# Optimization experiments

Hardware: AMD Instinct MI355X
Metric: run time of the kernel (lower is better)

The kernel has to match this reference:

```python
import jax, jax.numpy as jnp
import numpy as np

HID = 32      # STGAT hidden_dim
HEADS = 8
NHID = HID // HEADS  # per-head hidden = 4
NEG_SLOPE = 0.2


def lstm_layer(x, Wih, Whh, bih, bhh):
    # x: (BN, T, H_in); torch gate order i, f, g, o
    BN = x.shape[0]
    H = Whh.shape[1]
    b = bih + bhh

    def step(carry, xt):
        h, c = carry
        z = xt @ Wih.T + h @ Whh.T + b
        i, f, g, o = jnp.split(z, 4, axis=-1)
        c = jax.nn.sigmoid(f) * c + jax.nn.sigmoid(i) * jnp.tanh(g)
        h = jax.nn.sigmoid(o) * jnp.tanh(c)
        return (h, c), h

    h0 = jnp.zeros((BN, H), x.dtype)
    _, ys = jax.lax.scan(step, (h0, h0), jnp.swapaxes(x, 0, 1))
    return jnp.swapaxes(ys, 0, 1)  # (BN, T, H)


def setup_inputs():
    key = jax.random.key(0)
    ks = jax.random.split(key, 16)
    B, N, T_in, F_in = 8, 300, 12, 3
    T_out, F_out = 12, 3
    X = jax.random.normal(ks[0], (B, N, T_in, F_in), jnp.float32)
    adj = (jax.random.uniform(ks[1], (N, N)) < 0.05).astype(jnp.float32)
    A_hat = jnp.maximum(adj, jnp.eye(N, dtype=jnp.float32))  # self-loops

    def init(k, shape, fan):
        return jax.random.normal(k, shape, jnp.float32) / np.float32(np.sqrt(fan))

    W_gat = init(ks[2], (HID, F_in), F_in)          # linear (no bias)
    a_attn = init(ks[3], (2 * NHID,), 2 * NHID)     # attn (no bias), flattened (1, 2*nhid)
    W_ih0 = init(ks[4], (4 * HID, HID), HID)
    W_hh0 = init(ks[5], (4 * HID, HID), HID)
    b_ih0 = init(ks[6], (4 * HID,), HID)
    b_hh0 = init(ks[7], (4 * HID,), HID)
    W_ih1 = init(ks[8], (4 * HID, HID), HID)
    W_hh1 = init(ks[9], (4 * HID, HID), HID)
    b_ih1 = init(ks[10], (4 * HID,), HID)
    b_hh1 = init(ks[11], (4 * HID,), HID)
    fc_W = init(ks[12], (F_out * T_out, HID), HID)
    fc_b = init(ks[13], (F_out * T_out,), HID)
    return {"A_hat": A_hat, "X": X, "W_gat": W_gat, "a_attn": a_attn,
            "W_ih0": W_ih0, "W_hh0": W_hh0, "b_ih0": b_ih0, "b_hh0": b_hh0,
            "W_ih1": W_ih1, "W_hh1": W_hh1, "b_ih1": b_ih1, "b_hh1": b_hh1,
            "fc_W": fc_W, "fc_b": fc_b}


def reference(A_hat, X, W_gat, a_attn, W_ih0, W_hh0, b_ih0, b_hh0,
              W_ih1, W_hh1, b_ih1, b_hh1, fc_W, fc_b):
    B, N, T, F = X.shape
    T_out = fc_W.shape[0] // F  # nums_feature_output == F here

    # --- GAT, vectorized over (batch, timestep) ---
    # g: (B, N, T, HEADS, NHID)
    g = (X @ W_gat.T).reshape(B, N, T, HEADS, NHID)
    a_l, a_r = a_attn[:NHID], a_attn[NHID:]
    # attn(g_concat) = a_l . g_i + a_r . g_j  (exact split of the concat+linear)
    gl = jnp.einsum('bithd,d->bith', g, a_l)
    gr = jnp.einsum('bjthd,d->bjth', g, a_r)
    e = jax.nn.leaky_relu(gl[:, :, None] + gr[:, None, :], NEG_SLOPE)  # (B,i,j,T,H)
    mask = (A_hat == 0)[None, :, :, None, None]
    e = jnp.where(mask, -jnp.inf, e)
    a = jax.nn.softmax(e, axis=2)  # softmax over j (dim=1 of the (i,j,h) tensor)
    h_gat = jnp.einsum('bijth,bjthd->bithd', a, g).reshape(B, N, T, HID)

    # --- 2-layer LSTM over time, per (b, n) sequence ---
    lstm_in = h_gat.reshape(B * N, T, HID)
    h1 = lstm_layer(lstm_in, W_ih0, W_hh0, b_ih0, b_hh0)
    h2 = lstm_layer(h1, W_ih1, W_hh1, b_ih1, b_hh1)
    h_last = h2[:, -1, :]  # (B*N, HID)

    out = h_last @ fc_W.T + fc_b
    return out.reshape(B, N, T_out, F)
```

## Files before the change

kernel.cpp:

```cpp
#include <hip/hip_runtime.h>

typedef __attribute__((ext_vector_type(8))) short s8v;
typedef __attribute__((ext_vector_type(4))) float f4v;

__device__ __forceinline__ float sgm(float x) { return 1.f / (1.f + __expf(-x)); }
__device__ __forceinline__ float tanh_fast(float x) {
    float e = __expf(-2.f * fabsf(x));
    float t = (1.f - e) / (1.f + e);
    return copysignf(t, x);
}
__device__ __forceinline__ void bsplit(float x, short& hi, short& lo) {
    unsigned u = __float_as_uint(x);
    unsigned hb = u & 0xffff0000u;
    hi = (short)(hb >> 16);
    float r = x - __uint_as_float(hb);
    lo = (short)(__float_as_uint(r) >> 16);
}

__global__ void k_nbr(const float* __restrict__ A, const float* __restrict__ Wg,
                      const float* __restrict__ aat,
                      int* __restrict__ cnt, int* __restrict__ idx,
                      float* __restrict__ walr)
{
    int i = blockIdx.x;
    int lane = threadIdx.x;
    if (i == 0 && lane < 48) {
        int h = lane / 6, q = lane - h*6;
        int cc = q % 3; bool right = q >= 3;
        float acc = 0.f;
        #pragma unroll
        for (int dd = 0; dd < 4; dd++)
            acc += aat[right ? 4+dd : dd] * Wg[(h*4+dd)*3 + cc];
        walr[lane] = acc;
    }
    int c = 0;
    for (int j0 = 0; j0 < 300; j0 += 64) {
        int j = j0 + lane;
        bool p = (j < 300) && (A[i*300 + j] != 0.f);
        unsigned long long m = __ballot(p);
        if (p) {
            int pos = __popcll(m & ((1ull << lane) - 1ull));
            if (c + pos < 64) idx[i*64 + c + pos] = j;
        }
        c += __popcll(m);
    }
    if (c > 64) c = 64;
    if (lane == 0) cnt[i] = c;
}

__global__ __launch_bounds__(256, 4) void k_attn2(
    const float* __restrict__ X, const float* __restrict__ Wg,
    const int* __restrict__ cnt, const int* __restrict__ idx,
    const float* __restrict__ walr, float* __restrict__ hgat)
{
    int u = blockIdx.x * 4 + (threadIdx.x >> 6);
    int lane = threadIdx.x & 63;
    int h = lane >> 3, j8 = lane & 7, d = j8 & 3;
    int seq = u / 12, t = u - seq*12;
    int b = seq / 300, i = seq - b*300;

    const float* wv = walr + h*6;
    float wal0 = wv[0], wal1 = wv[1], wal2 = wv[2];
    float war0 = wv[3], war1 = wv[4], war2 = wv[5];
    const float* wp = Wg + (h*4+d)*3;
    float wp0 = wp[0], wp1 = wp[1], wp2 = wp[2];

    int c = cnt[i];
    int jj[8];
    #pragma unroll
    for (int q = 0; q < 8; q++) jj[q] = idx[i*64 + q*8 + j8];

    const float* Xb = X + (size_t)b*300*36 + t*3;
    const float* Xi = Xb + i*36;
    float x0 = Xi[0], x1 = Xi[1], x2 = Xi[2];
    float gl = x0*wal0 + x1*wal1 + x2*wal2;

    float m = -1e30f, s = 0.f, a0 = 0.f, a1 = 0.f, a2 = 0.f;
    for (int q = 0; q*8 + j8 < c; q++) {
        int j = jj[q];
        const float* Xj = Xb + j*36;
        float y0 = Xj[0], y1 = Xj[1], y2 = Xj[2];
        float e = gl + y0*war0 + y1*war1 + y2*war2;
        e = e > 0.f ? e : 0.2f*e;
        if (e > m) {
            float sc = __expf(m - e);
            s = s*sc + 1.f;
            a0 = a0*sc + y0; a1 = a1*sc + y1; a2 = a2*sc + y2;
            m = e;
        } else {
            float w = __expf(e - m);
            s += w;
            a0 += w*y0; a1 += w*y1; a2 += w*y2;
        }
    }
    #pragma unroll
    for (int off = 1; off <= 4; off <<= 1) {
        float m2 = __shfl_xor(m, off, 64);
        float s2 = __shfl_xor(s, off, 64);
        float b0 = __shfl_xor(a0, off, 64);
        float b1 = __shfl_xor(a1, off, 64);
        float b2 = __shfl_xor(a2, off, 64);
        float mo = fmaxf(m, m2);
        float w1 = __expf(m - mo), w2 = __expf(m2 - mo);
        s = s*w1 + s2*w2;
        a0 = a0*w1 + b0*w2; a1 = a1*w1 + b1*w2; a2 = a2*w1 + b2*w2;
        m = mo;
    }
    if (j8 < 4) {
        float o = (a0*wp0 + a1*wp1 + a2*wp2) / s;
        hgat[(size_t)u*32 + h*4 + d] = o;
    }
}

#define SQ 10

__device__ __forceinline__ void zcomp(const short* vh, const short* vl,
    const s8v (&ah)[2], const s8v (&al)[2], f4v bias, float* zdst,
    int boff, int g, int w, int n16)
{
    s8v bh0 = *(const s8v*)((const char*)vh + boff +      g*16);
    s8v bh1 = *(const s8v*)((const char*)vh + boff + 64 + g*16);
    s8v bl0 = *(const s8v*)((const char*)vl + boff +      g*16);
    s8v bl1 = *(const s8v*)((const char*)vl + boff + 64 + g*16);
    f4v acc = bias;
    acc = __builtin_amdgcn_mfma_f32_16x16x32_bf16(ah[0], bh0, acc, 0, 0, 0);
    acc = __builtin_amdgcn_mfma_f32_16x16x32_bf16(ah[1], bh1, acc, 0, 0, 0);
    acc = __builtin_amdgcn_mfma_f32_16x16x32_bf16(al[0], bh0, acc, 0, 0, 0);
    acc = __builtin_amdgcn_mfma_f32_16x16x32_bf16(al[1], bh1, acc, 0, 0, 0);
    acc = __builtin_amdgcn_mfma_f32_16x16x32_bf16(ah[0], bl0, acc, 0, 0, 0);
    acc = __builtin_amdgcn_mfma_f32_16x16x32_bf16(ah[1], bl1, acc, 0, 0, 0);
    *(f4v*)&zdst[n16*132 + w*16 + g*4] = acc;
}

__device__ __forceinline__ float cellupd(const float* zbp, int us, int uc, float& cst)
{
    float zi = zbp[us*132 + uc],      zf = zbp[us*132 + 32 + uc];
    float zg = zbp[us*132 + 64 + uc], zo = zbp[us*132 + 96 + uc];
    cst = sgm(zf)*cst + sgm(zi)*tanh_fast(zg);
    return sgm(zo)*tanh_fast(cst);
}

__global__ __launch_bounds__(512, 1) void k_lstm5(
    const float* __restrict__ hgat,
    const float* __restrict__ Wih0, const float* __restrict__ Whh0,
    const float* __restrict__ bih0, const float* __restrict__ bhh0,
    const float* __restrict__ Wih1, const float* __restrict__ Whh1,
    const float* __restrict__ bih1, const float* __restrict__ bhh1,
    const float* __restrict__ fcW,  const float* __restrict__ fcb,
    float* __restrict__ out)
{
    __shared__ __align__(16) short vh0[16*72], vl0[16*72];
    __shared__ __align__(16) short vh1[16*72], vl1[16*72];
    __shared__ __align__(16) float zb0[16*132], zb1[16*132];
    __shared__ float sh1f[SQ*32];

    const int tid = threadIdx.x;
    const int w   = tid >> 6;
    const int l   = tid & 63;
    const int n16 = l & 15;
    const int g   = l >> 4;
    const int zrow = w*16 + n16;

    s8v a0h[2], a0l[2], a1h[2], a1l[2];
    {
        const float* s00 = Wih0 + zrow*32 + g*8;
        const float* s01 = Whh0 + zrow*32 + g*8;
        const float* s10 = Wih1 + zrow*32 + g*8;
        const float* s11 = Whh1 + zrow*32 + g*8;
        #pragma unroll
        for (int j = 0; j < 8; j++) {
            short hh, ll;
            bsplit(s00[j], hh, ll); a0h[0][j]=hh; a0l[0][j]=ll;
            bsplit(s01[j], hh, ll); a0h[1][j]=hh; a0l[1][j]=ll;
            bsplit(s10[j], hh, ll); a1h[0][j]=hh; a1l[0][j]=ll;
            bsplit(s11[j], hh, ll); a1h[1][j]=hh; a1l[1][j]=ll;
        }
    }
    f4v bias0, bias1;
    #pragma unroll
    for (int r = 0; r < 4; r++) {
        int rr = w*16 + g*4 + r;
        bias0[r] = bih0[rr] + bhh0[rr];
        bias1[r] = bih1[rr] + bhh1[rr];
    }

    const int us = tid >> 5, uc = tid & 31;
    const bool upd = tid < SQ*32;
    const int seq0 = blockIdx.x * SQ;
    const int boff = n16 * 144;

    if (upd) {
        short hh, ll;
        bsplit(hgat[(size_t)(seq0+us)*384 + uc], hh, ll);
        vh0[us*72 + uc] = hh;      vl0[us*72 + uc] = ll;
        vh0[us*72 + 32 + uc] = 0;  vl0[us*72 + 32 + uc] = 0;
        vh1[us*72 + uc] = 0;       vl1[us*72 + uc] = 0;
        vh1[us*72 + 32 + uc] = 0;  vl1[us*72 + 32 + uc] = 0;
    }
    __syncthreads();

    float c0 = 0.f, c1 = 0.f;

    zcomp(vh0, vl0, a0h, a0l, bias0, zb0, boff, g, w, n16);
    __syncthreads();
    if (upd) {
        float h0v = cellupd(zb0, us, uc, c0);
        short hh, ll; bsplit(h0v, hh, ll);
        vh0[us*72 + 32 + uc] = hh;  vl0[us*72 + 32 + uc] = ll;
        vh1[us*72 + uc]      = hh;  vl1[us*72 + uc]      = ll;
        bsplit(hgat[(size_t)(seq0+us)*384 + 32 + uc], hh, ll);
        vh0[us*72 + uc] = hh;  vl0[us*72 + uc] = ll;
    }
    __syncthreads();

    for (int t = 0; t < 12; t++) {
        zcomp(vh1, vl1, a1h, a1l, bias1, zb1, boff, g, w, n16);
        if (t < 11)
            zcomp(vh0, vl0, a0h, a0l, bias0, zb0, boff, g, w, n16);
        __syncthreads();
        if (upd) {
            float h1v = cellupd(zb1, us, uc, c1);
            short hh, ll; bsplit(h1v, hh, ll);
            vh1[us*72 + 32 + uc] = hh;  vl1[us*72 + 32 + uc] = ll;
            if (t == 11) sh1f[us*32 + uc] = h1v;
            if (t < 11) {
                float h0v = cellupd(zb0, us, uc, c0);
                bsplit(h0v, hh, ll);
                vh0[us*72 + 32 + uc] = hh;  vl0[us*72 + 32 + uc] = ll;
                vh1[us*72 + uc]      = hh;  vl1[us*72 + uc]      = ll;
                if (t + 2 < 12) {
                    bsplit(hgat[(size_t)(seq0+us)*384 + (t+2)*32 + uc], hh, ll);
                    vh0[us*72 + uc] = hh;  vl0[us*72 + uc] = ll;
                }
            }
        }
        __syncthreads();
    }

    if (tid < SQ*36) {
        int s = tid / 36, r = tid - s*36;
        float acc = fcb[r];
        #pragma unroll
        for (int c4 = 0; c4 < 8; c4++) {
            float4 uv = *(const float4*)&fcW[r*32 + 4*c4];
            acc += uv.x*sh1f[s*32+4*c4+0] + uv.y*sh1f[s*32+4*c4+1]
                 + uv.z*sh1f[s*32+4*c4+2] + uv.w*sh1f[s*32+4*c4+3];
        }
        out[(seq0 + s)*36 + r] = acc;
    }
}

__device__ __forceinline__ void lstm_step_fb(
    const float* __restrict__ sWi, const float* __restrict__ sWh,
    float bzi, float bzf, float bzg, float bzo,
    const float (&xf)[32], float (&hf)[32], float& cst, int k, int lb)
{
    float zi = bzi, zf = bzf, zg = bzg, zo = bzo;
    const int sw = k & 15;
    #pragma unroll
    for (int c2 = 0; c2 < 16; c2++) {
        const int col = 2 * (c2 ^ sw);
        float xa = xf[2*c2], xb = xf[2*c2+1];
        float ha = hf[2*c2], hb = hf[2*c2+1];
        float2 wiA = *(const float2*)&sWi[(0  + k)*32 + col];
        float2 whA = *(const float2*)&sWh[(0  + k)*32 + col];
        zi += wiA.x*xa + wiA.y*xb + whA.x*ha + whA.y*hb;
        float2 wiB = *(const float2*)&sWi[(32 + k)*32 + col];
        float2 whB = *(const float2*)&sWh[(32 + k)*32 + col];
        zf += wiB.x*xa + wiB.y*xb + whB.x*ha + whB.y*hb;
        float2 wiC = *(const float2*)&sWi[(64 + k)*32 + col];
        float2 whC = *(const float2*)&sWh[(64 + k)*32 + col];
        zg += wiC.x*xa + wiC.y*xb + whC.x*ha + whC.y*hb;
        float2 wiD = *(const float2*)&sWi[(96 + k)*32 + col];
        float2 whD = *(const float2*)&sWh[(96 + k)*32 + col];
        zo += wiD.x*xa + wiD.y*xb + whD.x*ha + whD.y*hb;
    }
    float ig = sgm(zi)*tanhf(zg);
    cst = sgm(zf)*cst + ig;
    float hl = sgm(zo)*tanhf(cst);
    #pragma unroll
    for (int d = 0; d < 32; d++) hf[d] = __shfl(hl, lb + d, 64);
}

__global__ __launch_bounds__(256) void k_fused_fb(
    const float* __restrict__ A,    const float* __restrict__ X,
    const float* __restrict__ Wg,   const float* __restrict__ aat,
    const float* __restrict__ Wih0, const float* __restrict__ Whh0,
    const float* __restrict__ bih0, const float* __restrict__ bhh0,
    const float* __restrict__ Wih1, const float* __restrict__ Whh1,
    const float* __restrict__ bih1, const float* __restrict__ bhh1,
    const float* __restrict__ fcW,  const float* __restrict__ fcb,
    float* __restrict__ out)
{
    __shared__ float sW0i[4096], sW0h[4096], sW1i[4096], sW1h[4096];
    const int tid = threadIdx.x;
    for (int x2 = tid; x2 < 2048; x2 += 256) {
        int r = x2 >> 4, p = x2 & 15;
        int o = r*32 + 2*(p ^ (r & 15));
        *(float2*)&sW0i[o] = *(const float2*)&Wih0[r*32 + 2*p];
        *(float2*)&sW0h[o] = *(const float2*)&Whh0[r*32 + 2*p];
        *(float2*)&sW1i[o] = *(const float2*)&Wih1[r*32 + 2*p];
        *(float2*)&sW1h[o] = *(const float2*)&Whh1[r*32 + 2*p];
    }
    const int w   = tid >> 5;
    const int k   = tid & 31;
    const int lb  = tid & 32;
    const int seq = blockIdx.x * 8 + w;
    const int b   = seq / 300, i = seq % 300;

    int nb0 = 0, nb1 = 0, cntv = 0;
    for (int j0 = 0; j0 < 300; j0 += 32) {
        int j = j0 + k;
        bool p = (j < 300) && (A[i*300 + j] != 0.f);
        unsigned long long m64 = __ballot(p);
        unsigned mm = (unsigned)(m64 >> lb);
        while (mm) {
            int bpos = __ffs(mm) - 1;
            if ((cntv & 31) == k && cntv < 64) {
                if (cntv & 32) nb1 = j0 + bpos; else nb0 = j0 + bpos;
            }
            cntv++;
            mm &= mm - 1;
        }
    }
    if (cntv > 64) cntv = 64;

    const int dd = k & 3;
    float wg0 = Wg[k*3+0], wg1 = Wg[k*3+1], wg2 = Wg[k*3+2];
    float alv = aat[dd],   arv = aat[4+dd];
    float b0i = bih0[k]    + bhh0[k];
    float b0f = bih0[32+k] + bhh0[32+k];
    float b0g = bih0[64+k] + bhh0[64+k];
    float b0o = bih0[96+k] + bhh0[96+k];
    float b1i = bih1[k]    + bhh1[k];
    float b1f = bih1[32+k] + bhh1[32+k];
    float b1g = bih1[64+k] + bhh1[64+k];
    float b1o = bih1[96+k] + bhh1[96+k];

    __syncthreads();

    float h0f[32], h1f[32];
    #pragma unroll
    for (int d = 0; d < 32; d++) { h0f[d] = 0.f; h1f[d] = 0.f; }
    float c0 = 0.f, c1 = 0.f;
    const size_t xrow = (size_t)(b*300 + i) * 36;

    for (int t = 0; t < 12; t++) {
        float gi = wg0*X[xrow + t*3 + 0] + wg1*X[xrow + t*3 + 1]
                 + wg2*X[xrow + t*3 + 2];
        float gl = gi * alv;
        gl += __shfl_xor(gl, 1, 64);
        gl += __shfl_xor(gl, 2, 64);

        float m = -1e30f, s = 0.f, acc = 0.f;
        for (int kk = 0; kk < cntv; kk++) {
            int v = (kk & 32) ? nb1 : nb0;
            int j = __shfl(v, lb + (kk & 31), 64);
            size_t xj = (size_t)(b*300 + j) * 36 + t*3;
            float gj = wg0*X[xj+0] + wg1*X[xj+1] + wg2*X[xj+2];
            float gr = gj * arv;
            gr += __shfl_xor(gr, 1, 64);
            gr += __shfl_xor(gr, 2, 64);
            float e = gl + gr;
            e = e > 0.f ? e : 0.2f*e;
            if (e > m) {
                float sc = __expf(m - e);
                s = s*sc + 1.f; acc = acc*sc + gj; m = e;
            } else {
                float wgt = __expf(e - m);
                s += wgt; acc += wgt*gj;
            }
        }
        float x_k = acc / s;
        float xf[32];
        #pragma unroll
        for (int d = 0; d < 32; d++) xf[d] = __shfl(x_k, lb + d, 64);
        lstm_step_fb(sW0i, sW0h, b0i, b0f, b0g, b0o, xf,  h0f, c0, k, lb);
        lstm_step_fb(sW1i, sW1h, b1i, b1f, b1g, b1o, h0f, h1f, c1, k, lb);
    }

    for (int r = k; r < 36; r += 32) {
        float a2 = fcb[r];
        #pragma unroll
        for (int c2 = 0; c2 < 16; c2++) {
            float2 u = *(const float2*)&fcW[r*32 + 2*c2];
            a2 += u.x*h1f[2*c2] + u.y*h1f[2*c2+1];
        }
        out[seq*36 + r] = a2;
    }
}

extern "C" void kernel_launch(void* const* d_in, const int* in_sizes, int n_in,
                              void* d_out, int out_size, void* d_ws, size_t ws_size,
                              hipStream_t stream)
{
    const float* A    = (const float*)d_in[0];
    const float* X    = (const float*)d_in[1];
    const float* Wg   = (const float*)d_in[2];
    const float* aat  = (const float*)d_in[3];
    const float* Wih0 = (const float*)d_in[4];
    const float* Whh0 = (const float*)d_in[5];
    const float* bih0 = (const float*)d_in[6];
    const float* bhh0 = (const float*)d_in[7];
    const float* Wih1 = (const float*)d_in[8];
    const float* Whh1 = (const float*)d_in[9];
    const float* bih1 = (const float*)d_in[10];
    const float* bhh1 = (const float*)d_in[11];
    const float* fcW  = (const float*)d_in[12];
    const float* fcb  = (const float*)d_in[13];
    float* out = (float*)d_out;

    const size_t need = (320 + 300*64) * sizeof(int) + 64*sizeof(float)
                      + (size_t)2400*384*sizeof(float);
    if (ws_size >= need) {
        int*   cnt  = (int*)d_ws;
        int*   idx  = cnt + 320;
        float* walr = (float*)(idx + 300*64);
        float* hgat = walr + 64;
        k_nbr  <<<300,  64,  0, stream>>>(A, Wg, aat, cnt, idx, walr);
        k_attn2<<<7200, 256, 0, stream>>>(X, Wg, cnt, idx, walr, hgat);
        k_lstm5<<<240,  512, 0, stream>>>(hgat, Wih0, Whh0, bih0, bhh0,
                                          Wih1, Whh1, bih1, bhh1, fcW, fcb, out);
    } else {
        k_fused_fb<<<300, 256, 0, stream>>>(A, X, Wg, aat,
                                            Wih0, Whh0, bih0, bhh0,
                                            Wih1, Whh1, bih1, bhh1,
                                            fcW, fcb, out);
    }
}
```

Baseline: 44.68 us.

## Fuse neighbor build, GAT attention and LSTM into one kernel

Merges the three launches (neighbor-list build, GAT attention, LSTM) into one 240-block kernel. Each block builds neighbor lists for its 10 sequences in shared memory and computes their GAT outputs into a shared buffer, then runs the MFMA LSTM on them. This removes two kernel launches and the global round-trip of the hgat intermediate. In exchange the GAT stage now runs on only 240 blocks instead of 7200 and recomputes neighbor lists redundantly across blocks. The workspace-free fallback kernel is also removed.

```diff
diff --git a/kernel.cpp b/kernel.cpp
--- a/kernel.cpp
+++ b/kernel.cpp
@@ -15,101 +15,6 @@
     hi = (short)(hb >> 16);
     float r = x - __uint_as_float(hb);
     lo = (short)(__float_as_uint(r) >> 16);
-}
-
-__global__ void k_nbr(const float* __restrict__ A, const float* __restrict__ Wg,
-                      const float* __restrict__ aat,
-                      int* __restrict__ cnt, int* __restrict__ idx,
-                      float* __restrict__ walr)
-{
-    int i = blockIdx.x;
-    int lane = threadIdx.x;
-    if (i == 0 && lane < 48) {
-        int h = lane / 6, q = lane - h*6;
-        int cc = q % 3; bool right = q >= 3;
-        float acc = 0.f;
-        #pragma unroll
-        for (int dd = 0; dd < 4; dd++)
-            acc += aat[right ? 4+dd : dd] * Wg[(h*4+dd)*3 + cc];
-        walr[lane] = acc;
-    }
-    int c = 0;
-    for (int j0 = 0; j0 < 300; j0 += 64) {
-        int j = j0 + lane;
-        bool p = (j < 300) && (A[i*300 + j] != 0.f);
-        unsigned long long m = __ballot(p);
-        if (p) {
-            int pos = __popcll(m & ((1ull << lane) - 1ull));
-            if (c + pos < 64) idx[i*64 + c + pos] = j;
-        }
-        c += __popcll(m);
-    }
-    if (c > 64) c = 64;
-    if (lane == 0) cnt[i] = c;
-}
-
-__global__ __launch_bounds__(256, 4) void k_attn2(
-    const float* __restrict__ X, const float* __restrict__ Wg,
-    const int* __restrict__ cnt, const int* __restrict__ idx,
-    const float* __restrict__ walr, float* __restrict__ hgat)
-{
-    int u = blockIdx.x * 4 + (threadIdx.x >> 6);
-    int lane = threadIdx.x & 63;
-    int h = lane >> 3, j8 = lane & 7, d = j8 & 3;
-    int seq = u / 12, t = u - seq*12;
-    int b = seq / 300, i = seq - b*300;
-
-    const float* wv = walr + h*6;
-    float wal0 = wv[0], wal1 = wv[1], wal2 = wv[2];
-    float war0 = wv[3], war1 = wv[4], war2 = wv[5];
-    const float* wp = Wg + (h*4+d)*3;
-    float wp0 = wp[0], wp1 = wp[1], wp2 = wp[2];
-
-    int c = cnt[i];
-    int jj[8];
-    #pragma unroll
-    for (int q = 0; q < 8; q++) jj[q] = idx[i*64 + q*8 + j8];
-
-    const float* Xb = X + (size_t)b*300*36 + t*3;
-    const float* Xi = Xb + i*36;
-    float x0 = Xi[0], x1 = Xi[1], x2 = Xi[2];
-    float gl = x0*wal0 + x1*wal1 + x2*wal2;
-
-    float m = -1e30f, s = 0.f, a0 = 0.f, a1 = 0.f, a2 = 0.f;
-    for (int q = 0; q*8 + j8 < c; q++) {
-        int j = jj[q];
-        const float* Xj = Xb + j*36;
-        float y0 = Xj[0], y1 = Xj[1], y2 = Xj[2];
-        float e = gl + y0*war0 + y1*war1 + y2*war2;
-        e = e > 0.f ? e : 0.2f*e;
-        if (e > m) {
-            float sc = __expf(m - e);
-            s = s*sc + 1.f;
-            a0 = a0*sc + y0; a1 = a1*sc + y1; a2 = a2*sc + y2;
-            m = e;
-        } else {
-            float w = __expf(e - m);
-            s += w;
-            a0 += w*y0; a1 += w*y1; a2 += w*y2;
-        }
-    }
-    #pragma unroll
-    for (int off = 1; off <= 4; off <<= 1) {
-        float m2 = __shfl_xor(m, off, 64);
-        float s2 = __shfl_xor(s, off, 64);
-        float b0 = __shfl_xor(a0, off, 64);
-        float b1 = __shfl_xor(a1, off, 64);
-        float b2 = __shfl_xor(a2, off, 64);
-        float mo = fmaxf(m, m2);
-        float w1 = __expf(m - mo), w2 = __expf(m2 - mo);
-        s = s*w1 + s2*w2;
-        a0 = a0*w1 + b0*w2; a1 = a1*w1 + b1*w2; a2 = a2*w1 + b2*w2;
-        m = mo;
-    }
-    if (j8 < 4) {
-        float o = (a0*wp0 + a1*wp1 + a2*wp2) / s;
-        hgat[(size_t)u*32 + h*4 + d] = o;
-    }
 }
 
 #define SQ 10
@@ -140,8 +45,9 @@
     return sgm(zo)*tanh_fast(cst);
 }
 
-__global__ __launch_bounds__(512, 1) void k_lstm5(
-    const float* __restrict__ hgat,
+__global__ __launch_bounds__(512, 1) void k_stgat(
+    const float* __restrict__ A,    const float* __restrict__ X,
+    const float* __restrict__ Wg,   const float* __restrict__ aat,
     const float* __restrict__ Wih0, const float* __restrict__ Whh0,
     const float* __restrict__ bih0, const float* __restrict__ bhh0,
     const float* __restrict__ Wih1, const float* __restrict__ Whh1,
@@ -149,18 +55,39 @@
     const float* __restrict__ fcW,  const float* __restrict__ fcb,
     float* __restrict__ out)
 {
+    __shared__ int   snbr[SQ][64];
+    __shared__ int   scnt[SQ];
+    __shared__ float shg[SQ*384];
     __shared__ __align__(16) short vh0[16*72], vl0[16*72];
     __shared__ __align__(16) short vh1[16*72], vl1[16*72];
     __shared__ __align__(16) float zb0[16*132], zb1[16*132];
     __shared__ float sh1f[SQ*32];
 
-    const int tid = threadIdx.x;
-    const int w   = tid >> 6;
-    const int l   = tid & 63;
-    const int n16 = l & 15;
-    const int g   = l >> 4;
+    const int tid  = threadIdx.x;
+    const int w    = tid >> 6;
+    const int l    = tid & 63;
+    const int seq0 = blockIdx.x * SQ;
+
+    for (int r = w; r < SQ; r += 8) {
+        int i = (seq0 + r) % 300;
+        int c = 0;
+        for (int j0 = 0; j0 < 300; j0 += 64) {
+            int j = j0 + l;
+            bool p = (j < 300) && (A[i*300 + j] != 0.f);
+            unsigned long long m = __ballot(p);
+            if (p) {
+                int pos = __popcll(m & ((1ull << l) - 1ull));
+                if (c + pos < 64) snbr[r][c + pos] = j;
+            }
+            c += __popcll(m);
+        }
+        if (c > 64) c = 64;
+        if (l == 0) scnt[r] = c;
+    }
+
+    const int n16  = l & 15;
+    const int g    = l >> 4;
     const int zrow = w*16 + n16;
-
     s8v a0h[2], a0l[2], a1h[2], a1l[2];
     {
         const float* s00 = Wih0 + zrow*32 + g*8;
@@ -184,14 +111,76 @@
         bias1[r] = bih1[rr] + bhh1[rr];
     }
 
+    __syncthreads();
+
+    {
+        const int h = l >> 3, j8 = l & 7, d = j8 & 3;
+        float wal0=0.f, wal1=0.f, wal2=0.f, war0=0.f, war1=0.f, war2=0.f;
+        #pragma unroll
+        for (int dd = 0; dd < 4; dd++) {
+            float av = aat[dd], bv = aat[4+dd];
+            const float* wr = Wg + (h*4+dd)*3;
+            wal0 += wr[0]*av; wal1 += wr[1]*av; wal2 += wr[2]*av;
+            war0 += wr[0]*bv; war1 += wr[1]*bv; war2 += wr[2]*bv;
+        }
+        const float* wp = Wg + (h*4+d)*3;
+        float wp0 = wp[0], wp1 = wp[1], wp2 = wp[2];
+
+        for (int q = 0; q < 15; q++) {
+            int u  = w*15 + q;
+            int us = u / 12, t = u - us*12;
+            int seq = seq0 + us;
+            int b = seq / 300, i = seq - b*300;
+            int c = scnt[us];
+
+            const float* Xb = X + (size_t)b*300*36 + t*3;
+            const float* Xi = Xb + i*36;
+            float gl = Xi[0]*wal0 + Xi[1]*wal1 + Xi[2]*wal2;
+
+            float m = -1e30f, s = 0.f, a0 = 0.f, a1 = 0.f, a2 = 0.f;
+            for (int kk = j8; kk < c; kk += 8) {
+                int j = snbr[us][kk];
+                const float* Xj = Xb + j*36;
+                float y0 = Xj[0], y1 = Xj[1], y2 = Xj[2];
+                float e = gl + y0*war0 + y1*war1 + y2*war2;
+                e = e > 0.f ? e : 0.2f*e;
+                if (e > m) {
+                    float sc = __expf(m - e);
+                    s = s*sc + 1.f;
+                    a0 = a0*sc + y0; a1 = a1*sc + y1; a2 = a2*sc + y2;
+                    m = e;
+                } else {
+                    float wt = __expf(e - m);
+                    s += wt;
+                    a0 += wt*y0; a1 += wt*y1; a2 += wt*y2;
+                }
+            }
+            #pragma unroll
+            for (int off = 1; off <= 4; off <<= 1) {
+                float m2 = __shfl_xor(m, off, 64);
+                float s2 = __shfl_xor(s, off, 64);
+                float b0 = __shfl_xor(a0, off, 64);
+                float b1 = __shfl_xor(a1, off, 64);
+                float b2 = __shfl_xor(a2, off, 64);
+                float mo = fmaxf(m, m2);
+                float w1 = __expf(m - mo), w2 = __expf(m2 - mo);
+                s = s*w1 + s2*w2;
+                a0 = a0*w1 + b0*w2; a1 = a1*w1 + b1*w2; a2 = a2*w1 + b2*w2;
+                m = mo;
+            }
+            if (j8 < 4)
+                shg[us*384 + t*32 + h*4 + d] = (a0*wp0 + a1*wp1 + a2*wp2) / s;
+        }
+    }
+    __syncthreads();
+
     const int us = tid >> 5, uc = tid & 31;
     const bool upd = tid < SQ*32;
-    const int seq0 = blockIdx.x * SQ;
     const int boff = n16 * 144;
 
     if (upd) {
         short hh, ll;
-        bsplit(hgat[(size_t)(seq0+us)*384 + uc], hh, ll);
+        bsplit(shg[us*384 + uc], hh, ll);
         vh0[us*72 + uc] = hh;      vl0[us*72 + uc] = ll;
         vh0[us*72 + 32 + uc] = 0;  vl0[us*72 + 32 + uc] = 0;
         vh1[us*72 + uc] = 0;       vl1[us*72 + uc] = 0;
@@ -208,7 +197,7 @@
         short hh, ll; bsplit(h0v, hh, ll);
         vh0[us*72 + 32 + uc] = hh;  vl0[us*72 + 32 + uc] = ll;
         vh1[us*72 + uc]      = hh;  vl1[us*72 + uc]      = ll;
-        bsplit(hgat[(size_t)(seq0+us)*384 + 32 + uc], hh, ll);
+        bsplit(shg[us*384 + 32 + uc], hh, ll);
         vh0[us*72 + uc] = hh;  vl0[us*72 + uc] = ll;
     }
     __syncthreads();
@@ -229,7 +218,7 @@
                 vh0[us*72 + 32 + uc] = hh;  vl0[us*72 + 32 + uc] = ll;
                 vh1[us*72 + uc]      = hh;  vl1[us*72 + uc]      = ll;
                 if (t + 2 < 12) {
-                    bsplit(hgat[(size_t)(seq0+us)*384 + (t+2)*32 + uc], hh, ll);
+                    bsplit(shg[us*384 + (t+2)*32 + uc], hh, ll);
                     vh0[us*72 + uc] = hh;  vl0[us*72 + uc] = ll;
                 }
             }
@@ -247,146 +236,6 @@
                  + uv.z*sh1f[s*32+4*c4+2] + uv.w*sh1f[s*32+4*c4+3];
         }
         out[(seq0 + s)*36 + r] = acc;
-    }
-}
-
-__device__ __forceinline__ void lstm_step_fb(
-    const float* __restrict__ sWi, const float* __restrict__ sWh,
-    float bzi, float bzf, float bzg, float bzo,
-    const float (&xf)[32], float (&hf)[32], float& cst, int k, int lb)
-{
-    float zi = bzi, zf = bzf, zg = bzg, zo = bzo;
-    const int sw = k & 15;
-    #pragma unroll
-    for (int c2 = 0; c2 < 16; c2++) {
-        const int col = 2 * (c2 ^ sw);
-        float xa = xf[2*c2], xb = xf[2*c2+1];
-        float ha = hf[2*c2], hb = hf[2*c2+1];
-        float2 wiA = *(const float2*)&sWi[(0  + k)*32 + col];
-        float2 whA = *(const float2*)&sWh[(0  + k)*32 + col];
-        zi += wiA.x*xa + wiA.y*xb + whA.x*ha + whA.y*hb;
-        float2 wiB = *(const float2*)&sWi[(32 + k)*32 + col];
-        float2 whB = *(const float2*)&sWh[(32 + k)*32 + col];
-        zf += wiB.x*xa + wiB.y*xb + whB.x*ha + whB.y*hb;
-        float2 wiC = *(const float2*)&sWi[(64 + k)*32 + col];
-        float2 whC = *(const float2*)&sWh[(64 + k)*32 + col];
-        zg += wiC.x*xa + wiC.y*xb + whC.x*ha + whC.y*hb;
-        float2 wiD = *(const float2*)&sWi[(96 + k)*32 + col];
-        float2 whD = *(const float2*)&sWh[(96 + k)*32 + col];
-        zo += wiD.x*xa + wiD.y*xb + whD.x*ha + whD.y*hb;
-    }
-    float ig = sgm(zi)*tanhf(zg);
-    cst = sgm(zf)*cst + ig;
-    float hl = sgm(zo)*tanhf(cst);
-    #pragma unroll
-    for (int d = 0; d < 32; d++) hf[d] = __shfl(hl, lb + d, 64);
-}
-
-__global__ __launch_bounds__(256) void k_fused_fb(
-    const float* __restrict__ A,    const float* __restrict__ X,
-    const float* __restrict__ Wg,   const float* __restrict__ aat,
-    const float* __restrict__ Wih0, const float* __restrict__ Whh0,
-    const float* __restrict__ bih0, const float* __restrict__ bhh0,
-    const float* __restrict__ Wih1, const float* __restrict__ Whh1,
-    const float* __restrict__ bih1, const float* __restrict__ bhh1,
-    const float* __restrict__ fcW,  const float* __restrict__ fcb,
-    float* __restrict__ out)
-{
-    __shared__ float sW0i[4096], sW0h[4096], sW1i[4096], sW1h[4096];
-    const int tid = threadIdx.x;
-    for (int x2 = tid; x2 < 2048; x2 += 256) {
-        int r = x2 >> 4, p = x2 & 15;
-        int o = r*32 + 2*(p ^ (r & 15));
-        *(float2*)&sW0i[o] = *(const float2*)&Wih0[r*32 + 2*p];
-        *(float2*)&sW0h[o] = *(const float2*)&Whh0[r*32 + 2*p];
-        *(float2*)&sW1i[o] = *(const float2*)&Wih1[r*32 + 2*p];
-        *(float2*)&sW1h[o] = *(const float2*)&Whh1[r*32 + 2*p];
-    }
-    const int w   = tid >> 5;
-    const int k   = tid & 31;
-    const int lb  = tid & 32;
-    const int seq = blockIdx.x * 8 + w;
-    const int b   = seq / 300, i = seq % 300;
-
-    int nb0 = 0, nb1 = 0, cntv = 0;
-    for (int j0 = 0; j0 < 300; j0 += 32) {
-        int j = j0 + k;
-        bool p = (j < 300) && (A[i*300 + j] != 0.f);
-        unsigned long long m64 = __ballot(p);
-        unsigned mm = (unsigned)(m64 >> lb);
-        while (mm) {
-            int bpos = __ffs(mm) - 1;
-            if ((cntv & 31) == k && cntv < 64) {
-                if (cntv & 32) nb1 = j0 + bpos; else nb0 = j0 + bpos;
-            }
-            cntv++;
-            mm &= mm - 1;
-        }
-    }
-    if (cntv > 64) cntv = 64;
-
-    const int dd = k & 3;
-    float wg0 = Wg[k*3+0], wg1 = Wg[k*3+1], wg2 = Wg[k*3+2];
-    float alv = aat[dd],   arv = aat[4+dd];
-    float b0i = bih0[k]    + bhh0[k];
-    float b0f = bih0[32+k] + bhh0[32+k];
-    float b0g = bih0[64+k] + bhh0[64+k];
-    float b0o = bih0[96+k] + bhh0[96+k];
-    float b1i = bih1[k]    + bhh1[k];
-    float b1f = bih1[32+k] + bhh1[32+k];
-    float b1g = bih1[64+k] + bhh1[64+k];
-    float b1o = bih1[96+k] + bhh1[96+k];
-
-    __syncthreads();
-
-    float h0f[32], h1f[32];
-    #pragma unroll
-    for (int d = 0; d < 32; d++) { h0f[d] = 0.f; h1f[d] = 0.f; }
-    float c0 = 0.f, c1 = 0.f;
-    const size_t xrow = (size_t)(b*300 + i) * 36;
-
-    for (int t = 0; t < 12; t++) {
-        float gi = wg0*X[xrow + t*3 + 0] + wg1*X[xrow + t*3 + 1]
-                 + wg2*X[xrow + t*3 + 2];
-        float gl = gi * alv;
-        gl += __shfl_xor(gl, 1, 64);
-        gl += __shfl_xor(gl, 2, 64);
-
-        float m = -1e30f, s = 0.f, acc = 0.f;
-        for (int kk = 0; kk < cntv; kk++) {
-            int v = (kk & 32) ? nb1 : nb0;
-            int j = __shfl(v, lb + (kk & 31), 64);
-            size_t xj = (size_t)(b*300 + j) * 36 + t*3;
-            float gj = wg0*X[xj+0] + wg1*X[xj+1] + wg2*X[xj+2];
-            float gr = gj * arv;
-            gr += __shfl_xor(gr, 1, 64);
-            gr += __shfl_xor(gr, 2, 64);
-            float e = gl + gr;
-            e = e > 0.f ? e : 0.2f*e;
-            if (e > m) {
-                float sc = __expf(m - e);
-                s = s*sc + 1.f; acc = acc*sc + gj; m = e;
-            } else {
-                float wgt = __expf(e - m);
-                s += wgt; acc += wgt*gj;
-            }
-        }
-        float x_k = acc / s;
-        float xf[32];
-        #pragma unroll
-        for (int d = 0; d < 32; d++) xf[d] = __shfl(x_k, lb + d, 64);
-        lstm_step_fb(sW0i, sW0h, b0i, b0f, b0g, b0o, xf,  h0f, c0, k, lb);
-        lstm_step_fb(sW1i, sW1h, b1i, b1f, b1g, b1o, h0f, h1f, c1, k, lb);
-    }
-
-    for (int r = k; r < 36; r += 32) {
-        float a2 = fcb[r];
-        #pragma unroll
-        for (int c2 = 0; c2 < 16; c2++) {
-            float2 u = *(const float2*)&fcW[r*32 + 2*c2];
-            a2 += u.x*h1f[2*c2] + u.y*h1f[2*c2+1];
-        }
-        out[seq*36 + r] = a2;
     }
 }
 
@@ -410,21 +259,8 @@
     const float* fcb  = (const float*)d_in[13];
     float* out = (float*)d_out;
 
-    const size_t need = (320 + 300*64) * sizeof(int) + 64*sizeof(float)
-                      + (size_t)2400*384*sizeof(float);
-    if (ws_size >= need) {
-        int*   cnt  = (int*)d_ws;
-        int*   idx  = cnt + 320;
-        float* walr = (float*)(idx + 300*64);
-        float* hgat = walr + 64;
-        k_nbr  <<<300,  64,  0, stream>>>(A, Wg, aat, cnt, idx, walr);
-        k_attn2<<<7200, 256, 0, stream>>>(X, Wg, cnt, idx, walr, hgat);
-        k_lstm5<<<240,  512, 0, stream>>>(hgat, Wih0, Whh0, bih0, bhh0,
-                                          Wih1, Whh1, bih1, bhh1, fcW, fcb, out);
-    } else {
-        k_fused_fb<<<300, 256, 0, stream>>>(A, X, Wg, aat,
-                                            Wih0, Whh0, bih0, bhh0,
-                                            Wih1, Whh1, bih1, bhh1,
-                                            fcW, fcb, out);
-    }
-}
+    k_stgat<<<240, 512, 0, stream>>>(A, X, Wg, aat,
+                                     Wih0, Whh0, bih0, bhh0,
+                                     Wih1, Whh1, bih1, bhh1,
+                                     fcW, fcb, out);
+}
```

New measurement: 44.00 us. Within noise of the previous version (-1.5%).
